# Kernel tuning notes

Measured on AMD Instinct MI355X. Metric: run time of the kernel, lower is better.

Reference implementation:

```python
import jax, jax.numpy as jnp
import numpy as np

DIM = 256
HEADS = 8
DIM_HEAD = 32
INNER = HEADS * DIM_HEAD  # 256
WH, WW = 8, 8
L, H, W = 2, 256, 256
SCALE = DIM_HEAD ** -0.5


def _relative_indices():
    # matches get_relative_distances + offset (window_size - 1)
    idx = np.array([[x, y] for x in range(WH) for y in range(WW)])  # [64, 2]
    dist = idx[None, :, :] - idx[:, None, :]                         # [64, 64, 2]
    return jnp.asarray(dist + np.array([WH - 1, WW - 1]), dtype=jnp.int32)


def setup_inputs() -> dict:
    key = jax.random.key(0)
    ks = jax.random.split(key, 5)
    x = jax.random.normal(ks[0], (L, H, W, DIM), dtype=jnp.float32)
    w_qkv = jax.random.normal(ks[1], (DIM, INNER * 3), dtype=jnp.float32) * (DIM ** -0.5)
    pos_emb = jax.random.normal(ks[2], (2 * WH - 1, 2 * WW - 1), dtype=jnp.float32)
    w_out = jax.random.normal(ks[3], (INNER, DIM), dtype=jnp.float32) * (INNER ** -0.5)
    b_out = jnp.zeros((DIM,), dtype=jnp.float32)
    rel_idx = _relative_indices()  # [64, 64, 2] int32
    return {"x": x, "w_qkv": w_qkv, "pos_emb": pos_emb, "w_out": w_out,
            "b_out": b_out, "rel_idx": rel_idx}


def _to_windows(t):
    # [L, H, W, INNER] -> [L, m, n_windows, window_tokens, dim_head]
    l = t.shape[0]
    nh, nw = H // WH, W // WW
    t = t.reshape(l, nh, WH, nw, WW, HEADS, DIM_HEAD)
    t = t.transpose(0, 5, 1, 3, 2, 4, 6)  # l, m, nh, nw, wh, ww, c
    return t.reshape(l, HEADS, nh * nw, WH * WW, DIM_HEAD)


def _from_windows(t):
    # inverse of _to_windows, merging heads back into channels
    l = t.shape[0]
    nh, nw = H // WH, W // WW
    t = t.reshape(l, HEADS, nh, nw, WH, WW, DIM_HEAD)
    t = t.transpose(0, 2, 4, 3, 5, 1, 6)  # l, nh, wh, nw, ww, m, c
    return t.reshape(l, H, W, INNER)


def reference(x, w_qkv, pos_emb, w_out, b_out, rel_idx):
    qkv = x @ w_qkv                              # [L, H, W, 3*INNER]
    q, k, v = jnp.split(qkv, 3, axis=-1)
    q, k, v = _to_windows(q), _to_windows(k), _to_windows(v)
    dots = jnp.einsum('lmhic,lmhjc->lmhij', q, k) * SCALE
    bias = pos_emb[rel_idx[:, :, 0], rel_idx[:, :, 1]]  # [64, 64]
    attn = jax.nn.softmax(dots + bias, axis=-1)
    out = jnp.einsum('lmhij,lmhjc->lmhic', attn, v)
    out = _from_windows(out)                      # [L, H, W, INNER]
    return out @ w_out + b_out
```

## Files before the change

kernel.cpp:

```cpp
#include <hip/hip_runtime.h>


typedef __bf16 bf16_t;
typedef __bf16 bf16x8 __attribute__((ext_vector_type(8)));
typedef __bf16 bf16x4 __attribute__((ext_vector_type(4)));
typedef float  f32x4  __attribute__((ext_vector_type(4)));

#define MFMA_BF16(a, b, c) __builtin_amdgcn_mfma_f32_16x16x32_bf16((a), (b), (c), 0, 0, 0)
#define SM_SCALE 0.17677669529663687f

#define WPK_OFF    0u
#define WOPK_OFF   393216u
#define BIASPC_OFF 524288u

__global__ __launch_bounds__(256) void prep_kernel(
    const float* __restrict__ w_qkv, const float* __restrict__ w_out,
    const float* __restrict__ pos_emb, const int* __restrict__ rel_idx,
    bf16_t* __restrict__ wpk, bf16_t* __restrict__ wopk,
    float* __restrict__ biasPC)
{
    int idx = blockIdx.x * 256 + threadIdx.x;
    if (idx < 196608) {
        int j = idx & 7, lane = (idx >> 3) & 63, t = idx >> 9;
        int ks = t & 7, ni = (t >> 3) & 1, hs = t >> 4;
        int s = hs % 3, h = hs / 3;
        int c = lane & 15, g = lane >> 4;
        int n = s * 256 + h * 32 + ni * 16 + c;
        int k = ks * 32 + g * 8 + j;
        wpk[idx] = (bf16_t)w_qkv[k * 768 + n];
    } else if (idx < 262144) {
        int t2 = idx - 196608;
        int j = t2 & 7, lane = (t2 >> 3) & 63, tt = t2 >> 9;
        int ks = tt & 7, nj = (tt >> 3) & 1, wv = tt >> 4;
        int c = lane & 15, g = lane >> 4;
        wopk[t2] = (bf16_t)w_out[(32 * ks + 8 * g + j) * 256 + 32 * wv + 16 * nj + c];
    } else if (idx < 266240) {
        int t = idx - 262144;
        int e = t >> 6, lane = t & 63;
        int ni = e >> 4, mi = (e >> 2) & 3, rg = e & 3;
        int i = 16 * ni + (lane & 15);
        int j = 16 * mi + 4 * (lane >> 4) + rg;
        int i0 = rel_idx[(i * 64 + j) * 2 + 0];
        int i1 = rel_idx[(i * 64 + j) * 2 + 1];
        biasPC[t] = pos_emb[i0 * 15 + i1];
    }
}

__global__ __launch_bounds__(512, 2) void fused_kernel(
    const float* __restrict__ x, const bf16_t* __restrict__ wpk,
    const float* __restrict__ biasPC, const bf16_t* __restrict__ wopk,
    const float* __restrict__ b_out, float* __restrict__ out)
{
    __shared__ __align__(16) bf16_t XA_s[64 * 256];
    __shared__ __align__(16) bf16_t SB_s[8][2560];

    const int tid = threadIdx.x;
    const int lane = tid & 63, wv = tid >> 6;
    const int g = lane >> 4, c = lane & 15;
    const int b = blockIdx.x;
    const int h = wv;
    const int rbase = (b >> 10) * 65536 + ((b >> 5) & 31) * 2048 + (b & 31) * 8;

    bf16_t* SB = SB_s[wv];
    f32x4 z4 = {0.f, 0.f, 0.f, 0.f};

    const bf16_t* wb0 = wpk + (size_t)(h * 3 + 0) * 8192;
    bf16x8 bfr[2][8];
#pragma unroll
    for (int ni = 0; ni < 2; ++ni)
#pragma unroll
        for (int ks = 0; ks < 8; ++ks)
            bfr[ni][ks] = *(const bf16x8*)(wb0 + (ni * 8 + ks) * 512 + lane * 8);

#pragma unroll
    for (int jj = 0; jj < 4; ++jj) {
        int q = jj * 512 + tid;
        int tok = q >> 5, ci = q & 31;
        int r = rbase + (tok >> 3) * 256 + (tok & 7);
        const f32x4* xp = (const f32x4*)(x + (size_t)r * 256 + ci * 8);
        f32x4 a = xp[0], bq = xp[1];
        bf16x8 t;
        t[0] = (bf16_t)a[0];  t[1] = (bf16_t)a[1];
        t[2] = (bf16_t)a[2];  t[3] = (bf16_t)a[3];
        t[4] = (bf16_t)bq[0]; t[5] = (bf16_t)bq[1];
        t[6] = (bf16_t)bq[2]; t[7] = (bf16_t)bq[3];
        *(bf16x8*)(XA_s + tok * 256 + ((ci ^ (tok & 31)) << 3)) = t;
    }
    __syncthreads();

    bf16x8 qf[4], kf[4], vbA[2][2];

#pragma unroll
    for (int s = 0; s < 3; ++s) {
        if (s > 0) {
            const bf16_t* wb = wpk + (size_t)(h * 3 + s) * 8192;
#pragma unroll
            for (int ni = 0; ni < 2; ++ni)
#pragma unroll
                for (int ks = 0; ks < 8; ++ks)
                    bfr[ni][ks] = *(const bf16x8*)(wb + (ni * 8 + ks) * 512 + lane * 8);
        }

        if (s < 2) {
            f32x4 acc[2][4];
#pragma unroll
            for (int i = 0; i < 2; ++i)
#pragma unroll
                for (int j = 0; j < 4; ++j) acc[i][j] = z4;
#pragma unroll
            for (int ks = 0; ks < 8; ++ks) {
                bf16x8 af[4];
#pragma unroll
                for (int mi = 0; mi < 4; ++mi) {
                    int tok = 16 * mi + c;
                    af[mi] = *(const bf16x8*)(XA_s + tok * 256 + (((4 * ks + g) ^ (tok & 31)) << 3));
                }
#pragma unroll
                for (int ni = 0; ni < 2; ++ni)
#pragma unroll
                    for (int mi = 0; mi < 4; ++mi)
                        acc[ni][mi] = MFMA_BF16(bfr[ni][ks], af[mi], acc[ni][mi]);
            }
#pragma unroll
            for (int mi = 0; mi < 4; ++mi)
#pragma unroll
                for (int ni = 0; ni < 2; ++ni) {
                    bf16x4 pk;
#pragma unroll
                    for (int rg = 0; rg < 4; ++rg)
                        pk[rg] = (bf16_t)acc[ni][mi][rg];
                    *(bf16x4*)(SB + (16 * mi + c) * 40 + 16 * ni + 4 * g) = pk;
                }
            if (s == 0) {
#pragma unroll
                for (int j = 0; j < 4; ++j)
                    qf[j] = *(const bf16x8*)(SB + (16 * j + c) * 40 + 8 * g);
            } else {
#pragma unroll
                for (int j = 0; j < 4; ++j)
                    kf[j] = *(const bf16x8*)(SB + (16 * j + c) * 40 + 8 * g);
            }
        } else {
            f32x4 acc[4][2];
#pragma unroll
            for (int i = 0; i < 4; ++i) { acc[i][0] = z4; acc[i][1] = z4; }
#pragma unroll
            for (int ks = 0; ks < 8; ++ks) {
                bf16x8 af[4];
#pragma unroll
                for (int mi = 0; mi < 4; ++mi) {
                    int tok = 16 * mi + c;
                    af[mi] = *(const bf16x8*)(XA_s + tok * 256 + (((4 * ks + g) ^ (tok & 31)) << 3));
                }
#pragma unroll
                for (int mi = 0; mi < 4; ++mi) {
                    acc[mi][0] = MFMA_BF16(af[mi], bfr[0][ks], acc[mi][0]);
                    acc[mi][1] = MFMA_BF16(af[mi], bfr[1][ks], acc[mi][1]);
                }
            }
#pragma unroll
            for (int mi = 0; mi < 4; ++mi)
#pragma unroll
                for (int ni = 0; ni < 2; ++ni) {
                    bf16x4 pk;
#pragma unroll
                    for (int rg = 0; rg < 4; ++rg)
                        pk[rg] = (bf16_t)acc[mi][ni][rg];
                    *(bf16x4*)(SB + (16 * ni + c) * 72 + 16 * mi + 4 * g) = pk;
                }
#pragma unroll
            for (int ks2 = 0; ks2 < 2; ++ks2) {
                vbA[ks2][0] = *(const bf16x8*)(SB + c * 72 + 32 * ks2 + 8 * g);
                vbA[ks2][1] = *(const bf16x8*)(SB + (16 + c) * 72 + 32 * ks2 + 8 * g);
            }
        }
    }
    __syncthreads();

    bf16_t* Pw = SB;
#pragma unroll
    for (int ni = 0; ni < 4; ++ni) {
        f32x4 s[4];
        __builtin_amdgcn_s_setprio(1);
#pragma unroll
        for (int mi = 0; mi < 4; ++mi)
            s[mi] = MFMA_BF16(kf[mi], qf[ni], z4);
        __builtin_amdgcn_s_setprio(0);

        float mx = -1e30f;
#pragma unroll
        for (int mi = 0; mi < 4; ++mi) {
#pragma unroll
            for (int rg = 0; rg < 4; ++rg) {
                float bb = biasPC[(ni * 16 + mi * 4 + rg) * 64 + lane];
                float t = fmaf(s[mi][rg], SM_SCALE, bb);
                s[mi][rg] = t;
                mx = fmaxf(mx, t);
            }
        }
        mx = fmaxf(mx, __shfl_xor(mx, 16));
        mx = fmaxf(mx, __shfl_xor(mx, 32));
        float sm = 0.f;
#pragma unroll
        for (int mi = 0; mi < 4; ++mi)
#pragma unroll
            for (int rg = 0; rg < 4; ++rg) {
                float p = __expf(s[mi][rg] - mx);
                s[mi][rg] = p;
                sm += p;
            }
        sm += __shfl_xor(sm, 16);
        sm += __shfl_xor(sm, 32);
        float inv = 1.0f / sm;

        bf16_t* Pl = Pw + (ni & 1) * 1024;
#pragma unroll
        for (int mi = 0; mi < 4; ++mi) {
            bf16x4 pk;
#pragma unroll
            for (int rg = 0; rg < 4; ++rg) pk[rg] = (bf16_t)s[mi][rg];
            *(bf16x4*)(Pl + c * 64 + (((2 * mi + (g >> 1)) ^ (c & 7)) << 3) + 4 * (g & 1)) = pk;
        }

        f32x4 o0 = z4, o1 = z4;
        __builtin_amdgcn_s_setprio(1);
#pragma unroll
        for (int ks = 0; ks < 2; ++ks) {
            bf16x8 pa = *(const bf16x8*)(Pl + c * 64 + (((4 * ks + g) ^ (c & 7)) << 3));
            o0 = MFMA_BF16(vbA[ks][0], pa, o0);
            o1 = MFMA_BF16(vbA[ks][1], pa, o1);
        }
        __builtin_amdgcn_s_setprio(0);
        int tok = 16 * ni + c;
#pragma unroll
        for (int mi = 0; mi < 2; ++mi) {
            f32x4 ov = (mi == 0) ? o0 : o1;
            bf16x4 pk;
#pragma unroll
            for (int rg = 0; rg < 4; ++rg) pk[rg] = (bf16_t)(ov[rg] * inv);
            int ci = h * 4 + mi * 2 + (g >> 1);
            *(bf16x4*)((char*)XA_s + tok * 512 + ((ci ^ (tok & 31)) << 4) + (g & 1) * 8) = pk;
        }
    }
    __syncthreads();

    f32x4 acc2[4][2];
#pragma unroll
    for (int i = 0; i < 4; ++i) { acc2[i][0] = z4; acc2[i][1] = z4; }

    const bf16_t* wo = wopk + (size_t)wv * 8192;
    for (int ks = 0; ks < 8; ++ks) {
        bf16x8 af2[4], bf2[2];
#pragma unroll
        for (int mi = 0; mi < 4; ++mi) {
            int rr = 16 * mi + c;
            af2[mi] = *(const bf16x8*)((char*)XA_s + rr * 512 + (((4 * ks + g) ^ (rr & 31)) << 4));
        }
#pragma unroll
        for (int nj = 0; nj < 2; ++nj)
            bf2[nj] = *(const bf16x8*)(wo + (nj * 8 + ks) * 512 + lane * 8);
#pragma unroll
        for (int mi = 0; mi < 4; ++mi)
#pragma unroll
            for (int nj = 0; nj < 2; ++nj)
                acc2[mi][nj] = MFMA_BF16(af2[mi], bf2[nj], acc2[mi][nj]);
    }

#pragma unroll
    for (int nj = 0; nj < 2; ++nj) {
        int gcol = 32 * wv + 16 * nj + c;
        float bo = b_out[gcol];
#pragma unroll
        for (int mi = 0; mi < 4; ++mi)
#pragma unroll
            for (int rg = 0; rg < 4; ++rg) {
                int tok = 16 * mi + 4 * g + rg;
                size_t r = (size_t)(rbase + (tok >> 3) * 256 + (tok & 7));
                out[r * 256 + gcol] = acc2[mi][nj][rg] + bo;
            }
    }
}

extern "C" void kernel_launch(void* const* d_in, const int* in_sizes, int n_in,
                              void* d_out, int out_size, void* d_ws, size_t ws_size,
                              hipStream_t stream) {
    const float* x       = (const float*)d_in[0];
    const float* w_qkv   = (const float*)d_in[1];
    const float* pos_emb = (const float*)d_in[2];
    const float* w_out   = (const float*)d_in[3];
    const float* b_out   = (const float*)d_in[4];
    const int*   rel_idx = (const int*)d_in[5];

    char* ws = (char*)d_ws;
    bf16_t* wpk    = (bf16_t*)(ws + WPK_OFF);
    bf16_t* wopk   = (bf16_t*)(ws + WOPK_OFF);
    float*  biasPC = (float*)(ws + BIASPC_OFF);
    float*  out    = (float*)d_out;

    prep_kernel<<<1040, 256, 0, stream>>>(w_qkv, w_out, pos_emb, rel_idx,
                                          wpk, wopk, biasPC);
    fused_kernel<<<2048, 512, 0, stream>>>(x, wpk, biasPC, wopk, b_out, out);
}
```

Measured before the change: 151.8 us.

## Fuse Q and K projections in one k-loop and raise occupancy hint

Q and K projections now share one k-loop that reads each X fragment from LDS once and streams the weight fragments from global memory per k-step, instead of preloading all 16 weight fragments into registers per projection. The V projection keeps the register preload. The launch-bounds minimum-blocks hint rises from 2 to 4 per CU to push the compiler toward fewer VGPRs. LDS use is about 72KB per block (64x256 bf16 plus 8x2560 bf16), so four 512-thread blocks may not fit on a CU. The tighter register cap risks spills, and per-step global weight loads add latency.

```diff
diff --git a/kernel.cpp b/kernel.cpp
--- a/kernel.cpp
+++ b/kernel.cpp
@@ -46,7 +46,7 @@
     }
 }
 
-__global__ __launch_bounds__(512, 2) void fused_kernel(
+__global__ __launch_bounds__(512, 4) void fused_kernel(
     const float* __restrict__ x, const bf16_t* __restrict__ wpk,
     const float* __restrict__ biasPC, const bf16_t* __restrict__ wopk,
     const float* __restrict__ b_out, float* __restrict__ out)
@@ -63,14 +63,6 @@
 
     bf16_t* SB = SB_s[wv];
     f32x4 z4 = {0.f, 0.f, 0.f, 0.f};
-
-    const bf16_t* wb0 = wpk + (size_t)(h * 3 + 0) * 8192;
-    bf16x8 bfr[2][8];
-#pragma unroll
-    for (int ni = 0; ni < 2; ++ni)
-#pragma unroll
-        for (int ks = 0; ks < 8; ++ks)
-            bfr[ni][ks] = *(const bf16x8*)(wb0 + (ni * 8 + ks) * 512 + lane * 8);
 
 #pragma unroll
     for (int jj = 0; jj < 4; ++jj) {
@@ -89,90 +81,100 @@
     __syncthreads();
 
     bf16x8 qf[4], kf[4], vbA[2][2];
-
-#pragma unroll
-    for (int s = 0; s < 3; ++s) {
-        if (s > 0) {
-            const bf16_t* wb = wpk + (size_t)(h * 3 + s) * 8192;
-#pragma unroll
-            for (int ni = 0; ni < 2; ++ni)
-#pragma unroll
-                for (int ks = 0; ks < 8; ++ks)
-                    bfr[ni][ks] = *(const bf16x8*)(wb + (ni * 8 + ks) * 512 + lane * 8);
-        }
-
-        if (s < 2) {
-            f32x4 acc[2][4];
-#pragma unroll
-            for (int i = 0; i < 2; ++i)
-#pragma unroll
-                for (int j = 0; j < 4; ++j) acc[i][j] = z4;
-#pragma unroll
-            for (int ks = 0; ks < 8; ++ks) {
-                bf16x8 af[4];
-#pragma unroll
-                for (int mi = 0; mi < 4; ++mi) {
-                    int tok = 16 * mi + c;
-                    af[mi] = *(const bf16x8*)(XA_s + tok * 256 + (((4 * ks + g) ^ (tok & 31)) << 3));
-                }
-#pragma unroll
-                for (int ni = 0; ni < 2; ++ni)
-#pragma unroll
-                    for (int mi = 0; mi < 4; ++mi)
-                        acc[ni][mi] = MFMA_BF16(bfr[ni][ks], af[mi], acc[ni][mi]);
-            }
-#pragma unroll
-            for (int mi = 0; mi < 4; ++mi)
-#pragma unroll
-                for (int ni = 0; ni < 2; ++ni) {
-                    bf16x4 pk;
-#pragma unroll
-                    for (int rg = 0; rg < 4; ++rg)
-                        pk[rg] = (bf16_t)acc[ni][mi][rg];
-                    *(bf16x4*)(SB + (16 * mi + c) * 40 + 16 * ni + 4 * g) = pk;
-                }
-            if (s == 0) {
-#pragma unroll
-                for (int j = 0; j < 4; ++j)
-                    qf[j] = *(const bf16x8*)(SB + (16 * j + c) * 40 + 8 * g);
-            } else {
-#pragma unroll
-                for (int j = 0; j < 4; ++j)
-                    kf[j] = *(const bf16x8*)(SB + (16 * j + c) * 40 + 8 * g);
-            }
-        } else {
-            f32x4 acc[4][2];
-#pragma unroll
-            for (int i = 0; i < 4; ++i) { acc[i][0] = z4; acc[i][1] = z4; }
-#pragma unroll
-            for (int ks = 0; ks < 8; ++ks) {
-                bf16x8 af[4];
-#pragma unroll
-                for (int mi = 0; mi < 4; ++mi) {
-                    int tok = 16 * mi + c;
-                    af[mi] = *(const bf16x8*)(XA_s + tok * 256 + (((4 * ks + g) ^ (tok & 31)) << 3));
-                }
-#pragma unroll
-                for (int mi = 0; mi < 4; ++mi) {
-                    acc[mi][0] = MFMA_BF16(af[mi], bfr[0][ks], acc[mi][0]);
-                    acc[mi][1] = MFMA_BF16(af[mi], bfr[1][ks], acc[mi][1]);
-                }
-            }
-#pragma unroll
-            for (int mi = 0; mi < 4; ++mi)
-#pragma unroll
-                for (int ni = 0; ni < 2; ++ni) {
-                    bf16x4 pk;
-#pragma unroll
-                    for (int rg = 0; rg < 4; ++rg)
-                        pk[rg] = (bf16_t)acc[mi][ni][rg];
-                    *(bf16x4*)(SB + (16 * ni + c) * 72 + 16 * mi + 4 * g) = pk;
-                }
-#pragma unroll
-            for (int ks2 = 0; ks2 < 2; ++ks2) {
-                vbA[ks2][0] = *(const bf16x8*)(SB + c * 72 + 32 * ks2 + 8 * g);
-                vbA[ks2][1] = *(const bf16x8*)(SB + (16 + c) * 72 + 32 * ks2 + 8 * g);
-            }
+    {
+        const bf16_t* wbq = wpk + (size_t)(h * 3 + 0) * 8192;
+        const bf16_t* wbk = wpk + (size_t)(h * 3 + 1) * 8192;
+        f32x4 accq[2][4], acck[2][4];
+#pragma unroll
+        for (int i = 0; i < 2; ++i)
+#pragma unroll
+            for (int j = 0; j < 4; ++j) { accq[i][j] = z4; acck[i][j] = z4; }
+
+#pragma unroll
+        for (int ks = 0; ks < 8; ++ks) {
+            bf16x8 bq0 = *(const bf16x8*)(wbq + ks * 512 + lane * 8);
+            bf16x8 bq1 = *(const bf16x8*)(wbq + (8 + ks) * 512 + lane * 8);
+            bf16x8 bk0 = *(const bf16x8*)(wbk + ks * 512 + lane * 8);
+            bf16x8 bk1 = *(const bf16x8*)(wbk + (8 + ks) * 512 + lane * 8);
+            bf16x8 af[4];
+#pragma unroll
+            for (int mi = 0; mi < 4; ++mi) {
+                int tok = 16 * mi + c;
+                af[mi] = *(const bf16x8*)(XA_s + tok * 256 + (((4 * ks + g) ^ (tok & 31)) << 3));
+            }
+#pragma unroll
+            for (int mi = 0; mi < 4; ++mi) {
+                accq[0][mi] = MFMA_BF16(bq0, af[mi], accq[0][mi]);
+                accq[1][mi] = MFMA_BF16(bq1, af[mi], accq[1][mi]);
+                acck[0][mi] = MFMA_BF16(bk0, af[mi], acck[0][mi]);
+                acck[1][mi] = MFMA_BF16(bk1, af[mi], acck[1][mi]);
+            }
+        }
+#pragma unroll
+        for (int mi = 0; mi < 4; ++mi)
+#pragma unroll
+            for (int ni = 0; ni < 2; ++ni) {
+                bf16x4 pk;
+#pragma unroll
+                for (int rg = 0; rg < 4; ++rg) pk[rg] = (bf16_t)accq[ni][mi][rg];
+                *(bf16x4*)(SB + (16 * mi + c) * 40 + 16 * ni + 4 * g) = pk;
+            }
+#pragma unroll
+        for (int j = 0; j < 4; ++j)
+            qf[j] = *(const bf16x8*)(SB + (16 * j + c) * 40 + 8 * g);
+#pragma unroll
+        for (int mi = 0; mi < 4; ++mi)
+#pragma unroll
+            for (int ni = 0; ni < 2; ++ni) {
+                bf16x4 pk;
+#pragma unroll
+                for (int rg = 0; rg < 4; ++rg) pk[rg] = (bf16_t)acck[ni][mi][rg];
+                *(bf16x4*)(SB + (16 * mi + c) * 40 + 16 * ni + 4 * g) = pk;
+            }
+#pragma unroll
+        for (int j = 0; j < 4; ++j)
+            kf[j] = *(const bf16x8*)(SB + (16 * j + c) * 40 + 8 * g);
+    }
+
+    {
+        const bf16_t* wb = wpk + (size_t)(h * 3 + 2) * 8192;
+        bf16x8 bfr[2][8];
+#pragma unroll
+        for (int ni = 0; ni < 2; ++ni)
+#pragma unroll
+            for (int ks = 0; ks < 8; ++ks)
+                bfr[ni][ks] = *(const bf16x8*)(wb + (ni * 8 + ks) * 512 + lane * 8);
+
+        f32x4 acc[4][2];
+#pragma unroll
+        for (int i = 0; i < 4; ++i) { acc[i][0] = z4; acc[i][1] = z4; }
+#pragma unroll
+        for (int ks = 0; ks < 8; ++ks) {
+            bf16x8 af[4];
+#pragma unroll
+            for (int mi = 0; mi < 4; ++mi) {
+                int tok = 16 * mi + c;
+                af[mi] = *(const bf16x8*)(XA_s + tok * 256 + (((4 * ks + g) ^ (tok & 31)) << 3));
+            }
+#pragma unroll
+            for (int mi = 0; mi < 4; ++mi) {
+                acc[mi][0] = MFMA_BF16(af[mi], bfr[0][ks], acc[mi][0]);
+                acc[mi][1] = MFMA_BF16(af[mi], bfr[1][ks], acc[mi][1]);
+            }
+        }
+#pragma unroll
+        for (int mi = 0; mi < 4; ++mi)
+#pragma unroll
+            for (int ni = 0; ni < 2; ++ni) {
+                bf16x4 pk;
+#pragma unroll
+                for (int rg = 0; rg < 4; ++rg) pk[rg] = (bf16_t)acc[mi][ni][rg];
+                *(bf16x4*)(SB + (16 * ni + c) * 72 + 16 * mi + 4 * g) = pk;
+            }
+#pragma unroll
+        for (int ks2 = 0; ks2 < 2; ++ks2) {
+            vbA[ks2][0] = *(const bf16x8*)(SB + c * 72 + 32 * ks2 + 8 * g);
+            vbA[ks2][1] = *(const bf16x8*)(SB + (16 + c) * 72 + 32 * ks2 + 8 * g);
         }
     }
     __syncthreads();
```

After: 169.4 us. 1.12x slower.
